# Performance work log

Measured on AMD Instinct MI355X. Metric: run time of the kernel, lower is better.

## Reference

```python
import jax, jax.numpy as jnp
import numpy as np

D = 256      # dim_model
H = 8        # n_head
FFN = 1024
L = 2        # n_layers
WIN = 100.0  # window_size of LocalisedEncoding
MINWL = 0.01 # min_wavelength of LocalisedEncoding
EPS = 1e-5


def _mass_sinusoid(mz):
    # depthcharge MassEncoder: min_wavelength=0.001, max_wavelength=10000
    n_sin = D // 2
    n_cos = D - n_sin
    base = 0.001 / (2.0 * np.pi)
    scale = 10000.0 / 0.001
    sin_term = (base * scale ** (np.arange(n_sin) / (n_sin - 1))).astype(np.float32)
    cos_term = (base * scale ** (np.arange(n_cos) / (n_cos - 1))).astype(np.float32)
    return jnp.concatenate([jnp.sin(mz / sin_term), jnp.cos(mz / cos_term)], axis=-1)


def _pe_lookup(pe, mass):
    # LocalisedEncoding.forward: clamp, linear index into precomputed table
    m = jnp.clip(mass, -WIN, WIN)
    idx = ((m + 1.0 + WIN) / MINWL).astype(jnp.int32)
    return pe[idx]


def _ln(x, g, b):
    mu = jnp.mean(x, axis=-1, keepdims=True)
    var = jnp.mean((x - mu) ** 2, axis=-1, keepdims=True)
    return (x - mu) * jax.lax.rsqrt(var + EPS) * g + b


def _forward(spectra, pe, latent, int_w, in_w, in_b, out_w, out_b,
             l1_w, l1_b, l2_w, l2_b, n1_g, n1_b, n2_g, n2_b):
    B, Np, _ = spectra.shape
    pad = jnp.sum(spectra, axis=2) == 0  # padded peaks
    # CustomPeakEncoder with mass=None, precursor_mass=None, dim_intensity=None
    peaks = _mass_sinusoid(spectra[:, :, :1]) + spectra[:, :, 1:2] @ int_w.T
    x = jnp.concatenate([jnp.broadcast_to(latent, (B, 1, D)), peaks], axis=1)
    mask = jnp.concatenate([jnp.zeros((B, 1), bool), pad], axis=1)  # [B,N]
    masses = jnp.concatenate([jnp.zeros((B, 1), spectra.dtype), spectra[:, :, 0]], axis=1)
    N = Np + 1
    hd = D // H
    scale = 1.0 / np.sqrt(hd)
    neg = jnp.asarray(-1e9, x.dtype)

    for l in range(L):
        wq, wk, wv = in_w[l, :D], in_w[l, D:2 * D], in_w[l, 2 * D:]
        bq, bk, bv = in_b[l, :D], in_b[l, D:2 * D], in_b[l, 2 * D:]
        if l == 0:
            # localized path: relative mass-difference encoding added to K/V
            pe0 = _pe_lookup(pe, jnp.zeros((), x.dtype))          # [D]
            q_in = x + pe0                                         # [B,N,D]
            rel = masses[:, None, :] - masses[:, :, None]          # m_j - m_i, [B,N,N]
            kv_in = x[:, None, :, :] + _pe_lookup(pe, rel)         # [B,N,N,D]
            Q = (q_in @ wq.T + bq).reshape(B, N, H, hd)
            K = (kv_in @ wk.T + bk).reshape(B, N, N, H, hd)
            V = (kv_in @ wv.T + bv).reshape(B, N, N, H, hd)
            s = jnp.einsum('bihd,bijhd->bhij', Q, K) * scale
            s = jnp.where(mask[:, None, None, :], neg, s)
            a = jax.nn.softmax(s, axis=-1)
            y = jnp.einsum('bhij,bijhd->bihd', a, V).reshape(B, N, D)
        else:
            Q = (x @ wq.T + bq).reshape(B, N, H, hd)
            K = (x @ wk.T + bk).reshape(B, N, H, hd)
            V = (x @ wv.T + bv).reshape(B, N, H, hd)
            s = jnp.einsum('bihd,bjhd->bhij', Q, K) * scale
            s = jnp.where(mask[:, None, None, :], neg, s)
            a = jax.nn.softmax(s, axis=-1)
            y = jnp.einsum('bhij,bjhd->bihd', a, V).reshape(B, N, D)
        y = y @ out_w[l].T + out_b[l]
        x = _ln(x + y, n1_g[l], n1_b[l])
        f = jax.nn.relu(x @ l1_w[l].T + l1_b[l]) @ l2_w[l].T + l2_b[l]
        x = _ln(x + f, n2_g[l], n2_b[l])
    return x


def setup_inputs() -> dict:
    key = jax.random.key(0)
    ks = jax.random.split(key, 14)
    B, Np = 16, 150
    mz = jax.random.uniform(ks[0], (B, Np, 1), dtype=jnp.float32) * 300.0
    inten = jax.random.uniform(ks[1], (B, Np, 1), dtype=jnp.float32)
    spectra = jnp.concatenate([mz, inten], axis=-1)
    # zero-pad the last 20 peaks of every other spectrum
    pad = (jnp.arange(Np)[None, :] >= 130) & (jnp.arange(B)[:, None] % 2 == 0)
    spectra = jnp.where(pad[:, :, None], 0.0, spectra)

    # LocalisedEncoding precomputed pe buffer (casanovo_style=True)
    max_len = int((WIN + 1) * 2 / MINWL)  # 20200
    pos = np.arange(max_len) - max_len // 2
    div = np.exp(np.arange(0, D, 2) * (-np.log(10000.0) / D))
    pe_np = np.zeros((max_len, D), np.float32)
    pe_np[:, : D // 2] = np.sin(pos[:, None] * div)
    pe_np[:, D // 2:] = np.cos(pos[:, None] * div)

    s = 0.05
    return {
        'spectra': spectra,
        'pe': jnp.asarray(pe_np),
        'latent': jax.random.normal(ks[2], (1, 1, D), jnp.float32) * s,
        'int_w': jax.random.normal(ks[3], (D, 1), jnp.float32) * s,
        'in_w': jax.random.normal(ks[4], (L, 3 * D, D), jnp.float32) * s,
        'in_b': jax.random.normal(ks[5], (L, 3 * D), jnp.float32) * s,
        'out_w': jax.random.normal(ks[6], (L, D, D), jnp.float32) * s,
        'out_b': jax.random.normal(ks[7], (L, D), jnp.float32) * s,
        'l1_w': jax.random.normal(ks[8], (L, FFN, D), jnp.float32) * s,
        'l1_b': jax.random.normal(ks[9], (L, FFN), jnp.float32) * s,
        'l2_w': jax.random.normal(ks[10], (L, D, FFN), jnp.float32) * s,
        'l2_b': jax.random.normal(ks[11], (L, D), jnp.float32) * s,
        'n1_g': jnp.ones((L, D), jnp.float32),
        'n1_b': jnp.zeros((L, D), jnp.float32),
        'n2_g': jnp.ones((L, D), jnp.float32),
        'n2_b': jnp.zeros((L, D), jnp.float32),
    }


def reference(spectra, pe, latent, int_w, in_w, in_b, out_w, out_b,
              l1_w, l1_b, l2_w, l2_b, n1_g, n1_b, n2_g, n2_b):
    return _forward(spectra, pe, latent, int_w, in_w, in_b, out_w, out_b,
                    l1_w, l1_b, l2_w, l2_b, n1_g, n1_b, n2_g, n2_b)
```

## Files before the change

### kernel.cpp

```cpp
#include <hip/hip_runtime.h>
#include <hip/hip_bf16.h>
#include <math.h>

#define BB 16
#define NP 150
#define NN 151
#define DD 256
#define HH 8
#define HD 32
#define FFN_ 1024
#define PE_LEN 20200
#define ROWS (BB*NN)
#define MPAD 2432
#define PE_PAD 20224
#define SQS 160


typedef __attribute__((ext_vector_type(8))) short short8;
typedef __attribute__((ext_vector_type(4))) float f32x4;
typedef __attribute__((ext_vector_type(4))) unsigned u32x4;

#if defined(__has_builtin)
#if __has_builtin(__builtin_amdgcn_fdot2_f32_bf16)
#define HAVE_DOT2 1
#endif
#endif
#ifndef HAVE_DOT2
#define HAVE_DOT2 0
#endif

__device__ __forceinline__ float r16(float x) {
    return __bfloat162float(__float2bfloat16(x));
}
__device__ __forceinline__ float us2f(unsigned short u) {
    return __uint_as_float((unsigned)u << 16);
}
__device__ __forceinline__ float lo2f(unsigned x) {
    return __uint_as_float(x << 16);
}
__device__ __forceinline__ float hi2f(unsigned x) {
    return __uint_as_float(x & 0xFFFF0000u);
}
__device__ __forceinline__ unsigned cvtpk(float lo, float hi) {
    unsigned r;
    asm("v_cvt_pk_bf16_f32 %0, %1, %2" : "=v"(r) : "v"(lo), "v"(hi));
    return r;
}
#if HAVE_DOT2
typedef __attribute__((ext_vector_type(2))) __bf16 bf16x2;
__device__ __forceinline__ float dot2bf(unsigned a, unsigned b, float acc) {
    bf16x2 av = __builtin_bit_cast(bf16x2, a);
    bf16x2 bv = __builtin_bit_cast(bf16x2, b);
    return __builtin_amdgcn_fdot2_f32_bf16(av, bv, acc, false);
}
#endif

#define PACK_BLOCKS 1024
__global__ __launch_bounds__(256) void buildpack_kernel(
    const float* __restrict__ spectra, const float* __restrict__ latent,
    const float* __restrict__ int_w, const float* __restrict__ pe,
    float* __restrict__ x, __hip_bfloat16* __restrict__ xb,
    __hip_bfloat16* __restrict__ xqb,
    float* __restrict__ masses, float* __restrict__ maskf,
    const float* __restrict__ in_w,  __hip_bfloat16* __restrict__ inw_p,
    const float* __restrict__ out_w, __hip_bfloat16* __restrict__ outw_p,
    const float* __restrict__ l1_w,  __hip_bfloat16* __restrict__ l1w_p,
    const float* __restrict__ l2_w,  __hip_bfloat16* __restrict__ l2w_p,
    __hip_bfloat16* __restrict__ pe_p)
{
    int tid = threadIdx.x;
    if (blockIdx.x < ROWS) {
        int bn = blockIdx.x;
        int b = bn / NN, n = bn % NN;
        float val;
        if (n == 0) {
            val = latent[tid];
            if (tid == 0) { masses[bn] = 0.0f; maskf[bn] = 0.0f; }
        } else {
            float mz = spectra[(b*NP + n - 1)*2 + 0];
            float it = spectra[(b*NP + n - 1)*2 + 1];
            int i = (tid < 128) ? tid : tid - 128;
            const double base_d = 0.001 / (2.0 * 3.141592653589793);
            double term_d = base_d * pow(1.0e7, (double)i / 127.0);
            float tf = (float)term_d;
            double arg = (double)mz / (double)tf;
            double sv = (tid < 128) ? sin(arg) : cos(arg);
            val = (float)sv + it * int_w[tid];
            if (tid == 0) {
                masses[bn] = mz;
                maskf[bn] = ((mz + it) == 0.0f) ? 1.0f : 0.0f;
            }
        }
        x[bn*DD + tid] = val;
        xb[bn*DD + tid] = __float2bfloat16(val);
        xqb[bn*DD + tid] = __float2bfloat16(val + pe[10100*DD + tid]);
    } else {
        long long base = (long long)(blockIdx.x - ROWS) * 256 + tid;
        const long long stride = (long long)PACK_BLOCKS * 256;
        for (long long i = base; i < (long long)PE_PAD*DD; i += stride)
            pe_p[i] = __float2bfloat16(i < (long long)PE_LEN*DD ? pe[i] : 0.0f);
        for (long long i = base; i < 2LL*768*DD; i += stride)
            inw_p[i] = __float2bfloat16(in_w[i]);
        for (long long i = base; i < 2LL*DD*DD; i += stride)
            outw_p[i] = __float2bfloat16(out_w[i]);
        for (long long i = base; i < 2LL*FFN_*DD; i += stride)
            l1w_p[i] = __float2bfloat16(l1_w[i]);
        for (long long i = base; i < 2LL*DD*FFN_; i += stride)
            l2w_p[i] = __float2bfloat16(l2_w[i]);
    }
}

template<typename CT>
__global__ __launch_bounds__(256) void gemm_mfma(
    const __hip_bfloat16* __restrict__ A, const __hip_bfloat16* __restrict__ W,
    const float* __restrict__ bias, CT* __restrict__ C,
    int M, int Nc, int K, int ldc, int relu)
{
    int wave = threadIdx.x >> 6;
    int lane = threadIdx.x & 63;
    int NT = Nc >> 5;
    int MT = (M + 31) >> 5;
    int id = blockIdx.x * 4 + wave;
    if (id >= MT * NT) return;
    int mt = id / NT, nt = id % NT;
    int m0 = mt * 32, n0 = nt * 32;
    int rl = lane & 15, q8 = (lane >> 4) * 8;

    const short8* Ap0 = (const short8*)(A + (size_t)(m0 + rl)*K + q8);
    const short8* Ap1 = (const short8*)(A + (size_t)(m0 + 16 + rl)*K + q8);
    const short8* Wp0 = (const short8*)(W + (size_t)(n0 + rl)*K + q8);
    const short8* Wp1 = (const short8*)(W + (size_t)(n0 + 16 + rl)*K + q8);

    f32x4 acc00 = {0,0,0,0}, acc01 = {0,0,0,0};
    f32x4 acc10 = {0,0,0,0}, acc11 = {0,0,0,0};
    int steps = K >> 5;
    for (int s = 0; s < steps; ++s) {
        short8 a0 = Ap0[s*4];
        short8 a1 = Ap1[s*4];
        short8 b0 = Wp0[s*4];
        short8 b1 = Wp1[s*4];
        acc00 = __builtin_amdgcn_mfma_f32_16x16x32_bf16(a0, b0, acc00, 0, 0, 0);
        acc01 = __builtin_amdgcn_mfma_f32_16x16x32_bf16(a0, b1, acc01, 0, 0, 0);
        acc10 = __builtin_amdgcn_mfma_f32_16x16x32_bf16(a1, b0, acc10, 0, 0, 0);
        acc11 = __builtin_amdgcn_mfma_f32_16x16x32_bf16(a1, b1, acc11, 0, 0, 0);
    }

    int rbase = (lane >> 4) * 4;
    #pragma unroll
    for (int sm = 0; sm < 2; ++sm) {
        #pragma unroll
        for (int sn = 0; sn < 2; ++sn) {
            f32x4 a = (sm == 0) ? (sn == 0 ? acc00 : acc01)
                                : (sn == 0 ? acc10 : acc11);
            int gc = n0 + sn*16 + rl;
            float bv = bias ? r16(bias[gc]) : 0.0f;
            #pragma unroll
            for (int rg = 0; rg < 4; ++rg) {
                int gr = m0 + sm*16 + rbase + rg;
                if (gr < M) {
                    float val = r16(a[rg]);
                    if (bias) val = r16(val + bv);
                    if (relu) val = fmaxf(val, 0.0f);
                    C[(size_t)gr*ldc + gc] = (CT)val;
                }
            }
        }
    }
}

template<int K>
__global__ __launch_bounds__(256) void gemm_skinny(
    const __hip_bfloat16* __restrict__ A, const __hip_bfloat16* __restrict__ W,
    const float* __restrict__ bias, float* __restrict__ C,
    int M, int Nc, int ldc)
{
    int NT = Nc >> 5;
    int id = blockIdx.x;
    int mt = id / NT, nt = id % NT;
    int m0 = mt * 16, n0 = nt * 32;
    int wave = threadIdx.x >> 6;
    int lane = threadIdx.x & 63;
    int rl = lane & 15, q8 = (lane >> 4) * 8;
    const int K4 = K >> 2;
    int k0 = wave * K4;

    const short8* Ap  = (const short8*)(A + (size_t)(m0 + rl)*K + k0 + q8);
    const short8* Wp0 = (const short8*)(W + (size_t)(n0 + rl)*K + k0 + q8);
    const short8* Wp1 = (const short8*)(W + (size_t)(n0 + 16 + rl)*K + k0 + q8);

    f32x4 acc0 = {0,0,0,0}, acc1 = {0,0,0,0};
    #pragma unroll
    for (int s = 0; s < K4/32; ++s) {
        short8 a  = Ap[s*4];
        short8 b0 = Wp0[s*4];
        short8 b1 = Wp1[s*4];
        acc0 = __builtin_amdgcn_mfma_f32_16x16x32_bf16(a, b0, acc0, 0, 0, 0);
        acc1 = __builtin_amdgcn_mfma_f32_16x16x32_bf16(a, b1, acc1, 0, 0, 0);
    }

    __shared__ float red[4][8][65];
    #pragma unroll
    for (int rg = 0; rg < 4; ++rg) {
        red[wave][rg][lane]   = acc0[rg];
        red[wave][4+rg][lane] = acc1[rg];
    }
    __syncthreads();

    #pragma unroll
    for (int t = 0; t < 2; ++t) {
        int sl = wave*2 + t;
        float s = red[0][sl][lane] + red[1][sl][lane]
                + red[2][sl][lane] + red[3][sl][lane];
        int rg = sl & 3, sn = sl >> 2;
        int gr = m0 + (lane >> 4)*4 + rg;
        int gc = n0 + sn*16 + rl;
        float val = r16(s);
        val = r16(val + r16(bias[gc]));
        if (gr < M) C[(size_t)gr*ldc + gc] = val;
    }
}

template<int QS, int KS>
__global__ __launch_bounds__(256) void gemm_sqk(
    const __hip_bfloat16* __restrict__ Q, const __hip_bfloat16* __restrict__ Kp,
    float* __restrict__ S)
{
    int wave = threadIdx.x >> 6;
    int lane = threadIdx.x & 63;
    int id = blockIdx.x * 4 + wave;
    if (id >= 16*8*100) return;
    int jt = id % 10, it = (id / 10) % 10;
    int h = (id / 100) & 7, b = id / 800;
    int i0 = it * 16, j0 = jt * 16;
    int rl = lane & 15, q8 = (lane >> 4) * 8;

    short8 a  = *(const short8*)(Q  + (size_t)(b*NN + i0 + rl)*QS + h*32 + q8);
    short8 kb = *(const short8*)(Kp + (size_t)(b*NN + j0 + rl)*KS + h*32 + q8);
    f32x4 acc = {0,0,0,0};
    acc = __builtin_amdgcn_mfma_f32_16x16x32_bf16(a, kb, acc, 0, 0, 0);

    float* Sb = S + ((size_t)(b*8 + h))*SQS*SQS;
    int rbase = (lane >> 4) * 4;
    #pragma unroll
    for (int rg = 0; rg < 4; ++rg) {
        int ii = i0 + rbase + rg, jj = j0 + rl;
        if (ii < NN && jj < NN)
            Sb[(size_t)ii*SQS + jj] = acc[rg];
    }
}

#define PEKV_BLK 632u
#define QKV0_BLK 456u

__device__ __forceinline__ void pekv_body(
    unsigned bid, int wave, int lane,
    const __hip_bfloat16* __restrict__ A, const __hip_bfloat16* __restrict__ W,
    __hip_bfloat16* __restrict__ C)
{
    const int K = 256, Nc = 512, ldc = 512, M = PE_LEN;
    int NT = Nc >> 5;
    int MT4 = (M + 127) >> 7;
    int id = bid * 4 + wave;
    if (id >= MT4 * NT) return;
    int mt = id / NT, nt = id % NT;
    int m0 = mt * 128, n0 = nt * 32;
    int rl = lane & 15, q8 = (lane >> 4) * 8;

    const short8* Ab  = (const short8*)(A + (size_t)(m0 + rl)*K + q8);
    const short8* Wp0 = (const short8*)(W + (size_t)(n0 + rl)*K + q8);
    const short8* Wp1 = (const short8*)(W + (size_t)(n0 + 16 + rl)*K + q8);
    const int rstep = K >> 3;

    f32x4 acc[4][2][2] = {};
    for (int s = 0; s < 8; ++s) {
        short8 b0 = Wp0[s*4];
        short8 b1 = Wp1[s*4];
        short8 a[4][2];
        #pragma unroll
        for (int t = 0; t < 4; ++t) {
            a[t][0] = Ab[(size_t)(t*32)*rstep + s*4];
            a[t][1] = Ab[(size_t)(t*32+16)*rstep + s*4];
        }
        #pragma unroll
        for (int t = 0; t < 4; ++t) {
            acc[t][0][0] = __builtin_amdgcn_mfma_f32_16x16x32_bf16(a[t][0], b0, acc[t][0][0], 0, 0, 0);
            acc[t][0][1] = __builtin_amdgcn_mfma_f32_16x16x32_bf16(a[t][0], b1, acc[t][0][1], 0, 0, 0);
            acc[t][1][0] = __builtin_amdgcn_mfma_f32_16x16x32_bf16(a[t][1], b0, acc[t][1][0], 0, 0, 0);
            acc[t][1][1] = __builtin_amdgcn_mfma_f32_16x16x32_bf16(a[t][1], b1, acc[t][1][1], 0, 0, 0);
        }
    }

    int rbase = (lane >> 4) * 4;
    #pragma unroll
    for (int t = 0; t < 4; ++t) {
        #pragma unroll
        for (int sm = 0; sm < 2; ++sm) {
            #pragma unroll
            for (int sn = 0; sn < 2; ++sn) {
                f32x4 a = acc[t][sm][sn];
                int gc = n0 + sn*16 + rl;
                #pragma unroll
                for (int rg = 0; rg < 4; ++rg) {
                    int gr = m0 + t*32 + sm*16 + rbase + rg;
                    if (gr < M)
                        C[(size_t)gr*ldc + gc] = (__hip_bfloat16)r16(a[rg]);
                }
            }
        }
    }
}

__device__ __forceinline__ void qkv0_body(
    unsigned bid, int wave, int lane,
    const __hip_bfloat16* __restrict__ xqb, const __hip_bfloat16* __restrict__ xb,
    const __hip_bfloat16* __restrict__ inw_p, const float* __restrict__ in_b,
    __hip_bfloat16* __restrict__ qb, __hip_bfloat16* __restrict__ kvb, int M)
{
    int MT = (M + 31) >> 5;
    int id = bid * 4 + wave;
    if (id >= MT * 24) return;
    int mt = id / 24, ntt = id % 24;
    bool isQ = (ntt < 8);
    const __hip_bfloat16* A = isQ ? xqb : xb;
    const __hip_bfloat16* W = inw_p + (isQ ? (size_t)ntt*32*DD
                                           : (size_t)(256 + (ntt-8)*32)*DD);
    const float* bias = in_b + (isQ ? ntt*32 : 256 + (ntt-8)*32);
    __hip_bfloat16* C = isQ ? qb : kvb;
    int ldc = isQ ? 256 : 512;
    int cbase = isQ ? ntt*32 : (ntt-8)*32;
    int m0 = mt * 32;
    int rl = lane & 15, q8 = (lane >> 4) * 8;
    const int K = DD;

    const short8* Ap0 = (const short8*)(A + (size_t)(m0 + rl)*K + q8);
    const short8* Ap1 = (const short8*)(A + (size_t)(m0 + 16 + rl)*K + q8);
    const short8* Wp0 = (const short8*)(W + (size_t)(rl)*K + q8);
    const short8* Wp1 = (const short8*)(W + (size_t)(16 + rl)*K + q8);

    f32x4 acc00 = {0,0,0,0}, acc01 = {0,0,0,0};
    f32x4 acc10 = {0,0,0,0}, acc11 = {0,0,0,0};
    for (int s = 0; s < K/32; ++s) {
        short8 a0 = Ap0[s*4];
        short8 a1 = Ap1[s*4];
        short8 b0 = Wp0[s*4];
        short8 b1 = Wp1[s*4];
        acc00 = __builtin_amdgcn_mfma_f32_16x16x32_bf16(a0, b0, acc00, 0, 0, 0);
        acc01 = __builtin_amdgcn_mfma_f32_16x16x32_bf16(a0, b1, acc01, 0, 0, 0);
        acc10 = __builtin_amdgcn_mfma_f32_16x16x32_bf16(a1, b0, acc10, 0, 0, 0);
        acc11 = __builtin_amdgcn_mfma_f32_16x16x32_bf16(a1, b1, acc11, 0, 0, 0);
    }

    int rbase = (lane >> 4) * 4;
    #pragma unroll
    for (int sm = 0; sm < 2; ++sm) {
        #pragma unroll
        for (int sn = 0; sn < 2; ++sn) {
            f32x4 a = (sm == 0) ? (sn == 0 ? acc00 : acc01)
                                : (sn == 0 ? acc10 : acc11);
            int gc = cbase + sn*16 + rl;
            float bv = r16(bias[sn*16 + rl]);
            #pragma unroll
            for (int rg = 0; rg < 4; ++rg) {
                int gr = m0 + sm*16 + rbase + rg;
                if (gr < M) {
                    float val = r16(a[rg]);
                    val = r16(val + bv);
                    C[(size_t)gr*ldc + gc] = (__hip_bfloat16)val;
                }
            }
        }
    }
}

__global__ __launch_bounds__(256) void pekv_qkv0_kernel(
    const __hip_bfloat16* __restrict__ pe_p, const __hip_bfloat16* __restrict__ wkv0,
    __hip_bfloat16* __restrict__ pekv,
    const __hip_bfloat16* __restrict__ xqb, const __hip_bfloat16* __restrict__ xb,
    const __hip_bfloat16* __restrict__ inw_p, const float* __restrict__ in_b,
    __hip_bfloat16* __restrict__ qb, __hip_bfloat16* __restrict__ kvb)
{
    int wave = threadIdx.x >> 6;
    int lane = threadIdx.x & 63;
    if (blockIdx.x < PEKV_BLK)
        pekv_body(blockIdx.x, wave, lane, pe_p, wkv0, pekv);
    else
        qkv0_body(blockIdx.x - PEKV_BLK, wave, lane, xqb, xb, inw_p, in_b,
                  qb, kvb, ROWS);
}

template<bool USE_PE, int QS, int VS>
__global__ __launch_bounds__(256) void attn_kernel(
    const __hip_bfloat16* __restrict__ qp,
    const __hip_bfloat16* __restrict__ vp,
    const __hip_bfloat16* __restrict__ pekv,
    const float* __restrict__ sqk,
    const float* __restrict__ masses, const float* __restrict__ maskf,
    __hip_bfloat16* __restrict__ yb)
{
    int b = blockIdx.x & 15;
    int i = blockIdx.x >> 4;
    int tid = threadIdx.x;
    int c = tid & 31;
    int g = tid >> 5;
    int h = c >> 2;
    const float scale = 0.17677669529663687f;

    __shared__ float sc[HH][152];
    __shared__ float msh[152];
    __shared__ int   tj[152];
    __shared__ __align__(16) float part[8][264];

    if (tid < NN) {
        float mval = maskf[b*NN + tid];
        msh[tid] = mval;
        if (USE_PE) {
            double m = (double)masses[b*NN + tid] - (double)masses[b*NN + i];
            m = fmin(fmax(m, -100.0), 100.0);
            tj[tid] = (int)(((m + 1.0) + 100.0) / 0.01);
        }
        const float* Sb = sqk + ((size_t)(b*8))*SQS*SQS + (size_t)i*SQS + tid;
        if (USE_PE) {
            #pragma unroll
            for (int hh = 0; hh < 8; ++hh)
                sc[hh][tid] = Sb[(size_t)hh*SQS*SQS];
        } else {
            #pragma unroll
            for (int hh = 0; hh < 8; ++hh) {
                float s = Sb[(size_t)hh*SQS*SQS] * scale;
                sc[hh][tid] = (mval != 0.0f) ? -1e9f : s;
            }
        }
    }

    unsigned qw[4];
#if !HAVE_DOT2
    float qf[8];
#endif
    if (USE_PE) {
        const u32x4 q4 = *(const u32x4*)((const unsigned short*)qp
                            + (size_t)(b*NN + i)*QS + c*8);
        qw[0] = q4[0]; qw[1] = q4[1]; qw[2] = q4[2]; qw[3] = q4[3];
#if !HAVE_DOT2
        #pragma unroll
        for (int w = 0; w < 4; ++w) { qf[2*w] = lo2f(qw[w]); qf[2*w+1] = hi2f(qw[w]); }
#endif
    }
    __syncthreads();

    const unsigned short* vbase = (const unsigned short*)vp + (size_t)(b*NN)*VS + c*8;
    const unsigned short* pkb = (const unsigned short*)pekv + c*8;
    const unsigned short* pvb = (const unsigned short*)pekv + 256 + c*8;

    if (USE_PE) {
        int j = g;
        u32x4 pcur = *(const u32x4*)(pkb + (size_t)tj[j]*512);
        for (int p = 0; p < 19; ++p) {
            int jn = j + 8;
            bool more = (jn < NN);
            u32x4 pn;
            if (more) pn = *(const u32x4*)(pkb + (size_t)tj[jn]*512);
            float acc = 0.0f;
#if HAVE_DOT2
            #pragma unroll
            for (int w = 0; w < 4; ++w) acc = dot2bf(qw[w], pcur[w], acc);
#else
            #pragma unroll
            for (int w = 0; w < 4; ++w) {
                acc = fmaf(qf[2*w],   lo2f(pcur[w]), acc);
                acc = fmaf(qf[2*w+1], hi2f(pcur[w]), acc);
            }
#endif
            acc += __shfl_xor(acc, 1);
            acc += __shfl_xor(acc, 2);
            if ((c & 3) == 0) {
                float s = (sc[h][j] + acc) * scale;
                if (msh[j] != 0.0f) s = -1e9f;
                sc[h][j] = s;
            }
            if (!more) break;
            j = jn; pcur = pn;
        }
        __syncthreads();
    }

    {
        int lane = tid & 31;
        int hh = g;
        float mx = -INFINITY;
        for (int j = lane; j < NN; j += 32) mx = fmaxf(mx, sc[hh][j]);
        #pragma unroll
        for (int off = 16; off; off >>= 1) mx = fmaxf(mx, __shfl_xor(mx, off, 32));
        float sum = 0.0f;
        for (int j = lane; j < NN; j += 32) {
            float e = expf(sc[hh][j] - mx);
            sc[hh][j] = e;
            sum += e;
        }
        #pragma unroll
        for (int off = 16; off; off >>= 1) sum += __shfl_xor(sum, off, 32);
        float inv = 1.0f / sum;
        for (int j = lane; j < NN; j += 32) sc[hh][j] = r16(sc[hh][j] * inv);
    }
    __syncthreads();

    {
        float ya[8];
        #pragma unroll
        for (int u = 0; u < 8; ++u) ya[u] = 0.0f;

#if HAVE_DOT2
        u32x4 vA = *(const u32x4*)(vbase + (size_t)g*VS);
        u32x4 vB = *(const u32x4*)(vbase + (size_t)(g+8)*VS);
        u32x4 pA, pB;
        if (USE_PE) {
            pA = *(const u32x4*)(pvb + (size_t)tj[g]*512);
            pB = *(const u32x4*)(pvb + (size_t)tj[g+8]*512);
        }
        for (int t = 0; t < 9; ++t) {
            int jA = g + t*16, jB = jA + 8;
            u32x4 nvA, nvB, npA, npB;
            if (t < 8) {
                int nA = jA + 16, nB = jB + 16;
                nvA = *(const u32x4*)(vbase + (size_t)nA*VS);
                nvB = *(const u32x4*)(vbase + (size_t)nB*VS);
                if (USE_PE) {
                    npA = *(const u32x4*)(pvb + (size_t)tj[nA]*512);
                    npB = *(const u32x4*)(pvb + (size_t)tj[nB]*512);
                }
            }
            unsigned apair = cvtpk(sc[h][jA], sc[h][jB]);
            #pragma unroll
            for (int w = 0; w < 4; ++w) {
                unsigned lopair, hipair;
                if (USE_PE) {
                    float sA0 = lo2f(vA[w]) + lo2f(pA[w]);
                    float sA1 = hi2f(vA[w]) + hi2f(pA[w]);
                    float sB0 = lo2f(vB[w]) + lo2f(pB[w]);
                    float sB1 = hi2f(vB[w]) + hi2f(pB[w]);
                    lopair = cvtpk(sA0, sB0);
                    hipair = cvtpk(sA1, sB1);
                } else {
                    lopair = __builtin_amdgcn_perm(vB[w], vA[w], 0x05040100u);
                    hipair = __builtin_amdgcn_perm(vB[w], vA[w], 0x07060302u);
                }
                ya[2*w]   = dot2bf(apair, lopair, ya[2*w]);
                ya[2*w+1] = dot2bf(apair, hipair, ya[2*w+1]);
            }
            if (t < 8) {
                vA = nvA; vB = nvB;
                if (USE_PE) { pA = npA; pB = npB; }
            }
        }
        if (g + 144 < NN) {
            int jT = g + 144;
            u32x4 v = *(const u32x4*)(vbase + (size_t)jT*VS);
            u32x4 pq;
            if (USE_PE) pq = *(const u32x4*)(pvb + (size_t)tj[jT]*512);
            float aT = sc[h][jT];
            #pragma unroll
            for (int w = 0; w < 4; ++w) {
                float v0 = lo2f(v[w]), v1 = hi2f(v[w]);
                if (USE_PE) {
                    unsigned pk2 = cvtpk(v0 + lo2f(pq[w]), v1 + hi2f(pq[w]));
                    v0 = lo2f(pk2); v1 = hi2f(pk2);
                }
                ya[2*w]   = fmaf(aT, v0, ya[2*w]);
                ya[2*w+1] = fmaf(aT, v1, ya[2*w+1]);
            }
        }
#else
        int j = g;
        u32x4 vcur = *(const u32x4*)(vbase + (size_t)j*VS);
        u32x4 pcur;
        if (USE_PE) pcur = *(const u32x4*)(pvb + (size_t)tj[j]*512);
        float acur = sc[h][j];
        for (int p = 0; p < 19; ++p) {
            int jn = j + 8;
            bool more = (jn < NN);
            u32x4 vn, pn;
            float an = 0.0f;
            if (more) {
                vn = *(const u32x4*)(vbase + (size_t)jn*VS);
                if (USE_PE) pn = *(const u32x4*)(pvb + (size_t)tj[jn]*512);
                an = sc[h][jn];
            }
            #pragma unroll
            for (int w = 0; w < 4; ++w) {
                float v0 = lo2f(vcur[w]), v1 = hi2f(vcur[w]);
                if (USE_PE) {
                    v0 = r16(v0 + lo2f(pcur[w]));
                    v1 = r16(v1 + hi2f(pcur[w]));
                }
                ya[2*w]   = fmaf(acur, v0, ya[2*w]);
                ya[2*w+1] = fmaf(acur, v1, ya[2*w+1]);
            }
            if (!more) break;
            j = jn; vcur = vn; acur = an;
            if (USE_PE) pcur = pn;
        }
#endif
        f32x4* pp = (f32x4*)&part[g][c*8];
        pp[0] = f32x4{ya[0], ya[1], ya[2], ya[3]};
        pp[1] = f32x4{ya[4], ya[5], ya[6], ya[7]};
    }
    __syncthreads();

    {
        float s = part[0][tid];
        #pragma unroll
        for (int g2 = 1; g2 < 8; ++g2) s += part[g2][tid];
        yb[(size_t)(b*NN + i)*DD + tid] = __float2bfloat16(s);
    }
}

template<bool WRITE_B>
__global__ __launch_bounds__(256) void add_ln_kernel(
    const float* __restrict__ xin, const float* __restrict__ res,
    const float* __restrict__ g, const float* __restrict__ bb,
    float* __restrict__ xout, __hip_bfloat16* __restrict__ xbout)
{
    int r = blockIdx.x; int tid = threadIdx.x;
    float v = xin[r*DD + tid] + res[r*DD + tid];
    __shared__ float red[4];
    float s = v;
    #pragma unroll
    for (int off = 32; off; off >>= 1) s += __shfl_xor(s, off);
    if ((tid & 63) == 0) red[tid >> 6] = s;
    __syncthreads();
    float mu = (red[0] + red[1] + red[2] + red[3]) * (1.0f/256.0f);
    __syncthreads();
    float d = v - mu;
    float s2 = d*d;
    #pragma unroll
    for (int off = 32; off; off >>= 1) s2 += __shfl_xor(s2, off);
    if ((tid & 63) == 0) red[tid >> 6] = s2;
    __syncthreads();
    float var = (red[0] + red[1] + red[2] + red[3]) * (1.0f/256.0f);
    float out = d * (1.0f / sqrtf(var + 1e-5f)) * g[tid] + bb[tid];
    xout[r*DD + tid] = out;
    if (WRITE_B) xbout[r*DD + tid] = __float2bfloat16(out);
}

extern "C" void kernel_launch(void* const* d_in, const int* in_sizes, int n_in,
                              void* d_out, int out_size, void* d_ws, size_t ws_size,
                              hipStream_t stream)
{
    const float* spectra = (const float*)d_in[0];
    const float* pe      = (const float*)d_in[1];
    const float* latent  = (const float*)d_in[2];
    const float* int_w   = (const float*)d_in[3];
    const float* in_w    = (const float*)d_in[4];
    const float* in_b    = (const float*)d_in[5];
    const float* out_w   = (const float*)d_in[6];
    const float* out_b   = (const float*)d_in[7];
    const float* l1_w    = (const float*)d_in[8];
    const float* l1_b    = (const float*)d_in[9];
    const float* l2_w    = (const float*)d_in[10];
    const float* l2_b    = (const float*)d_in[11];
    const float* n1_g    = (const float*)d_in[12];
    const float* n1_b    = (const float*)d_in[13];
    const float* n2_g    = (const float*)d_in[14];
    const float* n2_b    = (const float*)d_in[15];

    float* x      = (float*)d_ws;
    float* y2     = x      + ROWS*DD;
    float* masses = y2     + ROWS*DD;
    float* maskf  = masses + ROWS;
    float* sqkb   = maskf  + ROWS;
    __hip_bfloat16* bp = (__hip_bfloat16*)(sqkb + (size_t)16*8*SQS*SQS);
    __hip_bfloat16* xb    = bp;  bp += (size_t)MPAD*DD;
    __hip_bfloat16* xqb   = bp;  bp += (size_t)MPAD*DD;
    __hip_bfloat16* qb    = bp;  bp += (size_t)MPAD*DD;
    __hip_bfloat16* kvb   = bp;  bp += (size_t)MPAD*768;
    __hip_bfloat16* yb    = bp;  bp += (size_t)MPAD*DD;
    __hip_bfloat16* f1b   = bp;  bp += (size_t)MPAD*FFN_;
    __hip_bfloat16* pekv  = bp;  bp += (size_t)PE_PAD*512;
    __hip_bfloat16* pe_p  = bp;  bp += (size_t)PE_PAD*DD;
    __hip_bfloat16* inw_p = bp;  bp += (size_t)2*768*DD;
    __hip_bfloat16* outw_p= bp;  bp += (size_t)2*DD*DD;
    __hip_bfloat16* l1w_p = bp;  bp += (size_t)2*FFN_*DD;
    __hip_bfloat16* l2w_p = bp;  bp += (size_t)2*DD*FFN_;

    dim3 blk(256);
    auto GG = [](int M, int Nc){ return dim3((unsigned)((((M+31)>>5)*(Nc>>5) + 3) / 4)); };
    const unsigned SK256 = (ROWS/16) * (256 >> 5);
    const unsigned SQKG  = (16*8*100 + 3) / 4;

    buildpack_kernel<<<ROWS + PACK_BLOCKS, blk, 0, stream>>>(
        spectra, latent, int_w, pe, x, xb, xqb, masses, maskf,
        in_w, inw_p, out_w, outw_p, l1_w, l1w_p, l2_w, l2w_p, pe_p);

    pekv_qkv0_kernel<<<PEKV_BLK + QKV0_BLK, blk, 0, stream>>>(
        pe_p, inw_p + 256*DD, pekv, xqb, xb, inw_p, in_b, qb, kvb);

    gemm_sqk<256,512><<<SQKG, blk, 0, stream>>>(qb, kvb, sqkb);
    attn_kernel<true,256,512><<<ROWS, blk, 0, stream>>>(
        qb, kvb + 256, pekv, sqkb, masses, maskf, yb);
    gemm_skinny<256><<<SK256, blk, 0, stream>>>(
        yb, outw_p, out_b, y2, ROWS, 256, 256);
    add_ln_kernel<true><<<ROWS, blk, 0, stream>>>(x, y2, n1_g, n1_b, x, xb);
    gemm_mfma<__hip_bfloat16><<<GG(ROWS, 1024), blk, 0, stream>>>(
        xb, l1w_p, l1_b, f1b, ROWS, 1024, 256, 1024, 1);
    gemm_skinny<1024><<<SK256, blk, 0, stream>>>(
        f1b, l2w_p, l2_b, y2, ROWS, 256, 256);
    add_ln_kernel<true><<<ROWS, blk, 0, stream>>>(x, y2, n2_g, n2_b, x, xb);

    gemm_mfma<__hip_bfloat16><<<GG(ROWS, 768), blk, 0, stream>>>(
        xb, inw_p + 768*DD, in_b + 768, kvb, ROWS, 768, 256, 768, 0);
    gemm_sqk<768,768><<<SQKG, blk, 0, stream>>>(kvb, kvb + 256, sqkb);
    attn_kernel<false,768,768><<<ROWS, blk, 0, stream>>>(
        kvb, kvb + 512, nullptr, sqkb, masses, maskf, yb);
    gemm_skinny<256><<<SK256, blk, 0, stream>>>(
        yb, outw_p + 256*DD, out_b + 256, y2, ROWS, 256, 256);
    add_ln_kernel<true><<<ROWS, blk, 0, stream>>>(x, y2, n1_g + 256, n1_b + 256, x, xb);
    gemm_mfma<__hip_bfloat16><<<GG(ROWS, 1024), blk, 0, stream>>>(
        xb, l1w_p + FFN_*DD, l1_b + 1024, f1b, ROWS, 1024, 256, 1024, 1);
    gemm_skinny<1024><<<SK256, blk, 0, stream>>>(
        f1b, l2w_p + DD*FFN_, l2_b + 256, y2, ROWS, 256, 256);
    add_ln_kernel<false><<<ROWS, blk, 0, stream>>>(x, y2, n2_g + 256, n2_b + 256,
                                                   (float*)d_out, nullptr);
}
```

Baseline: 302.8 us.

## Fuse attention output projection, residual add and LayerNorm into attention kernel

```diff
diff --git a/kernel.cpp b/kernel.cpp
--- a/kernel.cpp
+++ b/kernel.cpp
@@ -395,7 +395,10 @@
     const __hip_bfloat16* __restrict__ pekv,
     const float* __restrict__ sqk,
     const float* __restrict__ masses, const float* __restrict__ maskf,
-    __hip_bfloat16* __restrict__ yb)
+    const __hip_bfloat16* __restrict__ outw, const float* __restrict__ outb,
+    const float* __restrict__ xres,
+    const float* __restrict__ lng, const float* __restrict__ lnb,
+    float* __restrict__ xout, __hip_bfloat16* __restrict__ xbout)
 {
     int b = blockIdx.x & 15;
     int i = blockIdx.x >> 4;
@@ -409,6 +412,9 @@
     __shared__ float msh[152];
     __shared__ int   tj[152];
     __shared__ __align__(16) float part[8][264];
+    __shared__ float yrow[256];
+    __shared__ unsigned ypk[128];
+    __shared__ float red2[4];
 
     if (tid < NN) {
         float mval = maskf[b*NN + tid];
@@ -609,7 +615,61 @@
         float s = part[0][tid];
         #pragma unroll
         for (int g2 = 1; g2 < 8; ++g2) s += part[g2][tid];
-        yb[(size_t)(b*NN + i)*DD + tid] = __float2bfloat16(s);
+        yrow[tid] = s;
+    }
+    __syncthreads();
+    if (tid < 128) ypk[tid] = cvtpk(yrow[2*tid], yrow[2*tid + 1]);
+    __syncthreads();
+    {
+        const u32x4* W4 = (const u32x4*)((const unsigned short*)outw + (size_t)tid*DD);
+        float a0 = 0.0f, a1 = 0.0f, a2 = 0.0f, a3 = 0.0f;
+        #pragma unroll
+        for (int k = 0; k < 16; ++k) {
+            u32x4 w0 = W4[2*k];
+            u32x4 w1 = W4[2*k + 1];
+#if HAVE_DOT2
+            a0 = dot2bf(ypk[8*k+0], w0[0], a0);
+            a1 = dot2bf(ypk[8*k+1], w0[1], a1);
+            a2 = dot2bf(ypk[8*k+2], w0[2], a2);
+            a3 = dot2bf(ypk[8*k+3], w0[3], a3);
+            a0 = dot2bf(ypk[8*k+4], w1[0], a0);
+            a1 = dot2bf(ypk[8*k+5], w1[1], a1);
+            a2 = dot2bf(ypk[8*k+6], w1[2], a2);
+            a3 = dot2bf(ypk[8*k+7], w1[3], a3);
+#else
+            #pragma unroll
+            for (int u = 0; u < 4; ++u) {
+                unsigned yp0 = ypk[8*k+u], yp1 = ypk[8*k+4+u];
+                unsigned wd0 = w0[u], wd1 = w1[u];
+                a0 = fmaf(lo2f(yp0), lo2f(wd0), a0);
+                a1 = fmaf(hi2f(yp0), hi2f(wd0), a1);
+                a2 = fmaf(lo2f(yp1), lo2f(wd1), a2);
+                a3 = fmaf(hi2f(yp1), hi2f(wd1), a3);
+            }
+#endif
+        }
+        float val = r16((a0 + a1) + (a2 + a3));
+        val = r16(val + r16(outb[tid]));
+        size_t row = (size_t)(b*NN + i)*DD + tid;
+        float v = xres[row] + val;
+
+        float sr = v;
+        #pragma unroll
+        for (int off = 32; off; off >>= 1) sr += __shfl_xor(sr, off);
+        if ((tid & 63) == 0) red2[tid >> 6] = sr;
+        __syncthreads();
+        float mu = (red2[0] + red2[1] + red2[2] + red2[3]) * (1.0f/256.0f);
+        __syncthreads();
+        float dd = v - mu;
+        float s2 = dd*dd;
+        #pragma unroll
+        for (int off = 32; off; off >>= 1) s2 += __shfl_xor(s2, off);
+        if ((tid & 63) == 0) red2[tid >> 6] = s2;
+        __syncthreads();
+        float var = (red2[0] + red2[1] + red2[2] + red2[3]) * (1.0f/256.0f);
+        float out = dd * (1.0f / sqrtf(var + 1e-5f)) * lng[tid] + lnb[tid];
+        xout[row] = out;
+        xbout[row] = __float2bfloat16(out);
     }
 }
 
@@ -680,6 +740,7 @@
     __hip_bfloat16* outw_p= bp;  bp += (size_t)2*DD*DD;
     __hip_bfloat16* l1w_p = bp;  bp += (size_t)2*FFN_*DD;
     __hip_bfloat16* l2w_p = bp;  bp += (size_t)2*DD*FFN_;
+    (void)yb;
 
     dim3 blk(256);
     auto GG = [](int M, int Nc){ return dim3((unsigned)((((M+31)>>5)*(Nc>>5) + 3) / 4)); };
@@ -695,10 +756,8 @@
 
     gemm_sqk<256,512><<<SQKG, blk, 0, stream>>>(qb, kvb, sqkb);
     attn_kernel<true,256,512><<<ROWS, blk, 0, stream>>>(
-        qb, kvb + 256, pekv, sqkb, masses, maskf, yb);
-    gemm_skinny<256><<<SK256, blk, 0, stream>>>(
-        yb, outw_p, out_b, y2, ROWS, 256, 256);
-    add_ln_kernel<true><<<ROWS, blk, 0, stream>>>(x, y2, n1_g, n1_b, x, xb);
+        qb, kvb + 256, pekv, sqkb, masses, maskf,
+        outw_p, out_b, x, n1_g, n1_b, x, xb);
     gemm_mfma<__hip_bfloat16><<<GG(ROWS, 1024), blk, 0, stream>>>(
         xb, l1w_p, l1_b, f1b, ROWS, 1024, 256, 1024, 1);
     gemm_skinny<1024><<<SK256, blk, 0, stream>>>(
@@ -709,10 +768,8 @@
         xb, inw_p + 768*DD, in_b + 768, kvb, ROWS, 768, 256, 768, 0);
     gemm_sqk<768,768><<<SQKG, blk, 0, stream>>>(kvb, kvb + 256, sqkb);
     attn_kernel<false,768,768><<<ROWS, blk, 0, stream>>>(
-        kvb, kvb + 512, nullptr, sqkb, masses, maskf, yb);
-    gemm_skinny<256><<<SK256, blk, 0, stream>>>(
-        yb, outw_p + 256*DD, out_b + 256, y2, ROWS, 256, 256);
-    add_ln_kernel<true><<<ROWS, blk, 0, stream>>>(x, y2, n1_g + 256, n1_b + 256, x, xb);
+        kvb, kvb + 512, nullptr, sqkb, masses, maskf,
+        outw_p + 256*DD, out_b + 256, x, n1_g + 256, n1_b + 256, x, xb);
     gemm_mfma<__hip_bfloat16><<<GG(ROWS, 1024), blk, 0, stream>>>(
         xb, l1w_p + FFN_*DD, l1_b + 1024, f1b, ROWS, 1024, 256, 1024, 1);
     gemm_skinny<1024><<<SK256, blk, 0, stream>>>(
```

New measurement: 364.2 us. +20.3%, slower.
